# Kernel tuning notes

Measured on AMD Instinct MI355X. Metric: run time of the kernel, lower is better.

Reference implementation:

```python
import jax, jax.numpy as jnp
import numpy as np

H = 8  # number of heads


def setup_inputs() -> dict:
    key = jax.random.key(0)
    ks = jax.random.split(key, 7)
    B, L, D = 4, 2048, 512
    dh = D // H
    s = 1.0 / np.sqrt(D).astype(np.float32)
    return {
        "q": jax.random.normal(ks[0], (B, L, D), jnp.float32),
        "k": jax.random.normal(ks[1], (B, L, D), jnp.float32),
        "v": jax.random.normal(ks[2], (B, L, D), jnp.float32),
        "Wq": jax.random.normal(ks[3], (D, D), jnp.float32) * s,
        "Wk": jax.random.normal(ks[4], (D, D), jnp.float32) * s,
        "Wv": jax.random.normal(ks[5], (D, D), jnp.float32) * s,
        "E": jax.random.normal(ks[6], (L, dh), jnp.float32) * s,
    }


def _skew(QE):
    # QE: [B, H, L, L] -> pad one column on the left, reshape to [B,H,L+1,L],
    # drop the first row: the classic Music Transformer skewing trick.
    B, h, L, M = QE.shape
    padded = jnp.pad(QE, ((0, 0), (0, 0), (0, 0), (1, 0)))
    return padded.reshape(B, h, M + 1, L)[:, :, 1:, :]


def reference(q, k, v, Wq, Wk, Wv, E):
    B, L, D = q.shape
    dh = D // H

    def heads(x, W):
        return jnp.einsum('bld,de->ble', x, W).reshape(B, L, H, dh).transpose(0, 2, 1, 3)

    qh = heads(q, Wq)  # [B,H,L,dh]
    kh = heads(k, Wk)
    vh = heads(v, Wv)

    QE = jnp.einsum('bhld,md->bhlm', qh, E)      # [B,H,L,L]
    Srel = _skew(QE)                             # [B,H,L,L]
    QKt = jnp.einsum('bhld,bhmd->bhlm', qh, kh)  # [B,H,L,L]

    # NOTE: original divides AFTER softmax (faithful to source).
    attn = jax.nn.softmax(QKt + Srel, axis=-1) / float(np.sqrt(dh))
    out = jnp.einsum('bhlm,bhmd->bhld', attn, vh)
    return out.transpose(0, 2, 1, 3).reshape(B, L, D)
```

## Files before the change

### kernel.cpp

```cpp
#include <hip/hip_runtime.h>
#include <hip/hip_bf16.h>
#include <math.h>

typedef _Float16 f16;
typedef __attribute__((ext_vector_type(8))) _Float16 f16x8;
typedef __attribute__((ext_vector_type(4))) _Float16 f16x4;
typedef __attribute__((ext_vector_type(4))) float f32x4;

namespace {
constexpr int B = 4, L = 2048, D = 512, NH = 8, DH = 64;
}

__device__ __forceinline__ float dpp_xor1(float x) {
    return __int_as_float(__builtin_amdgcn_update_dpp(0, __float_as_int(x), 0xB1, 0xF, 0xF, true));
}
__device__ __forceinline__ float dpp_xor2(float x) {
    return __int_as_float(__builtin_amdgcn_update_dpp(0, __float_as_int(x), 0x4E, 0xF, 0xF, true));
}
__device__ __forceinline__ float dpp_ror4(float x) {
    return __int_as_float(__builtin_amdgcn_update_dpp(0, __float_as_int(x), 0x124, 0xF, 0xF, true));
}
__device__ __forceinline__ float dpp_ror8(float x) {
    return __int_as_float(__builtin_amdgcn_update_dpp(0, __float_as_int(x), 0x128, 0xF, 0xF, true));
}

__global__ __launch_bounds__(256)
void ecast_kernel(const float* __restrict__ E, f16* __restrict__ Ef) {
    int i4 = (blockIdx.x * 256 + threadIdx.x) * 4;
    float4 x = *(const float4*)(E + i4);
    *(f16x4*)(Ef + i4) = (f16x4){(f16)x.x, (f16)x.y, (f16)x.z, (f16)x.w};
}

__global__ __launch_bounds__(256)
void xcast_kernel(const float* __restrict__ q, const float* __restrict__ k,
                  const float* __restrict__ v, f16* __restrict__ Xf) {
    const int sel = blockIdx.y;
    const float* X = (sel == 0) ? q : (sel == 1) ? k : v;
    const size_t i4 = ((size_t)blockIdx.x * 256 + threadIdx.x) * 4;
    float4 x = *(const float4*)(X + i4);
    *(f16x4*)(Xf + (size_t)sel * ((size_t)B * L * D) + i4) =
        (f16x4){(f16)x.x, (f16)x.y, (f16)x.z, (f16)x.w};
}

__global__ __launch_bounds__(256)
void wtrans_kernel(const float* __restrict__ Wq, const float* __restrict__ Wk,
                   const float* __restrict__ Wv, f16* __restrict__ Wt) {
    __shared__ f16 Ws[64 * 65];
    const int sel = blockIdx.z;
    const float* W = (sel == 0) ? Wq : (sel == 1) ? Wk : Wv;
    f16* Wo = Wt + (size_t)sel * D * D;
    const int k0 = blockIdx.x * 64, n0 = blockIdx.y * 64;
    const int t = threadIdx.x;
#pragma unroll
    for (int i = 0; i < 16; ++i) {
        int idx = 256 * i + t;
        int r = idx >> 6, c = idx & 63;
        Ws[r * 65 + c] = (f16)W[(size_t)(k0 + r) * D + n0 + c];
    }
    __syncthreads();
    const int c = t >> 2, kseg = t & 3;
    f16x8 r0, r1;
#pragma unroll
    for (int j = 0; j < 8; ++j) r0[j] = Ws[(kseg * 16 + j) * 65 + c];
#pragma unroll
    for (int j = 0; j < 8; ++j) r1[j] = Ws[(kseg * 16 + 8 + j) * 65 + c];
    f16* o = Wo + (size_t)(n0 + c) * D + k0 + kseg * 16;
    *(f16x8*)o = r0;
    *(f16x8*)(o + 8) = r1;
}

__global__ __launch_bounds__(256, 4)
void proj_gemm(const f16* __restrict__ Xf, const f16* __restrict__ Wt,
               f16* __restrict__ Qf, f16* __restrict__ Kf, f16* __restrict__ Vtf) {
    __shared__ f16 As[128 * 72];
    __shared__ f16 Bs[64 * 72];
    const int flat = blockIdx.x;
    const int wg = (flat & 7) * 192 + (flat >> 3);
    const int by = wg % 24, bx = wg / 24;
    const int sel = by >> 3, h = by & 7;
    const int m0 = bx * 128;
    const f16* X = Xf + (size_t)sel * ((size_t)B * L * D);
    const f16* Bt = Wt + (size_t)sel * D * D + (size_t)h * 64 * D;
    const int t = threadIdx.x, wid = t >> 6, lane = t & 63;
    const int quad = lane >> 4, col = lane & 15;
    const int mw = wid * 32;

    f32x4 acc[2][4];
#pragma unroll
    for (int i = 0; i < 2; ++i)
#pragma unroll
        for (int j = 0; j < 4; ++j) acc[i][j] = (f32x4){0.f, 0.f, 0.f, 0.f};

    f16x8 xa[4];
    f16x8 breg[2];
    auto loadG = [&](int k0) {
#pragma unroll
        for (int i = 0; i < 4; ++i) {
            int idx = 256 * i + t;
            int r = idx >> 3, ch = idx & 7;
            xa[i] = *(const f16x8*)(X + (size_t)(m0 + r) * D + k0 + ch * 8);
        }
#pragma unroll
        for (int i = 0; i < 2; ++i) {
            int idx = 256 * i + t;
            int r = idx >> 3, ch = idx & 7;
            breg[i] = *(const f16x8*)(Bt + (size_t)r * D + k0 + ch * 8);
        }
    };
    auto storeL = [&]() {
#pragma unroll
        for (int i = 0; i < 4; ++i) {
            int idx = 256 * i + t;
            int r = idx >> 3, ch = idx & 7;
            *(f16x8*)(As + r * 72 + ch * 8) = xa[i];
        }
#pragma unroll
        for (int i = 0; i < 2; ++i) {
            int idx = 256 * i + t;
            int r = idx >> 3, ch = idx & 7;
            *(f16x8*)(Bs + r * 72 + ch * 8) = breg[i];
        }
    };

    loadG(0);
    for (int k0 = 0; k0 < D; k0 += 64) {
        __syncthreads();
        storeL();
        __syncthreads();
        if (k0 + 64 < D) loadG(k0 + 64);
#pragma unroll
        for (int ks = 0; ks < 2; ++ks) {
            f16x8 af[2], bf[4];
#pragma unroll
            for (int mt = 0; mt < 2; ++mt)
                af[mt] = *(const f16x8*)(As + (mw + mt * 16 + col) * 72 + quad * 8 + ks * 32);
#pragma unroll
            for (int nt = 0; nt < 4; ++nt)
                bf[nt] = *(const f16x8*)(Bs + (nt * 16 + col) * 72 + quad * 8 + ks * 32);
#pragma unroll
            for (int mt = 0; mt < 2; ++mt)
#pragma unroll
                for (int nt = 0; nt < 4; ++nt)
                    acc[mt][nt] = __builtin_amdgcn_mfma_f32_16x16x32_f16(af[mt], bf[nt], acc[mt][nt], 0, 0, 0);
        }
    }

    if (sel < 2) {
        f16* Y = (sel == 0) ? Qf : Kf;
#pragma unroll
        for (int mt = 0; mt < 2; ++mt)
#pragma unroll
            for (int nt = 0; nt < 4; ++nt)
#pragma unroll
                for (int reg = 0; reg < 4; ++reg) {
                    int m = m0 + mw + mt * 16 + quad * 4 + reg;
                    int bb = m >> 11, l = m & 2047, d = nt * 16 + col;
                    Y[((size_t)(bb * NH + h) * L + l) * DH + d] = (f16)acc[mt][nt][reg];
                }
    } else {
        __syncthreads();
        f16* Cs = As;
#pragma unroll
        for (int mt = 0; mt < 2; ++mt)
#pragma unroll
            for (int nt = 0; nt < 4; ++nt)
#pragma unroll
                for (int reg = 0; reg < 4; ++reg) {
                    int d = nt * 16 + col;
                    int lc = mw + mt * 16 + quad * 4 + reg;
                    Cs[d * 136 + lc] = (f16)acc[mt][nt][reg];
                }
        __syncthreads();
        const int dd = t >> 2, seg = t & 3;
        const int bb = m0 >> 11, l0 = m0 & 2047;
        f16* Yv = Vtf + ((size_t)(bb * NH + h) * DH + dd) * L + l0 + seg * 32;
#pragma unroll
        for (int j = 0; j < 4; ++j)
            *(f16x8*)(Yv + j * 8) = *(const f16x8*)(Cs + dd * 136 + seg * 32 + j * 8);
    }
}

__global__ __launch_bounds__(256, 4)
void attn_kernel(const f16* __restrict__ Qf, const f16* __restrict__ Kf,
                 const f16* __restrict__ Vtf, const f16* __restrict__ Ef,
                 float* __restrict__ out) {
    __shared__ f16 KfS[64 * 72];
    __shared__ f16 VfS[64 * 72];
    __shared__ f16 Pbuf[4][16 * 72];

    const int t = threadIdx.x, wid = t >> 6, lane = t & 63;
    const int quad = lane >> 4, col = lane & 15;
    const int l0w = blockIdx.x * 64 + wid * 16;
    const int h = blockIdx.y, bb = blockIdx.z;
    const size_t head = (size_t)(bb * NH + h) * (size_t)(L * DH);
    const f16* qf = Qf + head;
    const f16* kf = Kf + head;
    const f16* vt = Vtf + head;
    f16* Pw = Pbuf[wid];

    const f16x8 ones8 = {(f16)1.f, (f16)1.f, (f16)1.f, (f16)1.f,
                         (f16)1.f, (f16)1.f, (f16)1.f, (f16)1.f};

    f16x8 qF[2], qS[2];
    {
        const int m = l0w + col;
        const int mS = min(m + 1, L - 1);
#pragma unroll
        for (int ks = 0; ks < 2; ++ks) {
            const int off = quad * 8 + ks * 32;
            qF[ks] = *(const f16x8*)(qf + (size_t)m * DH + off);
            qS[ks] = *(const f16x8*)(qf + (size_t)mS * DH + off);
        }
    }

    f16x8 kreg[2], vreg[2];
    auto loadKV = [&](int c0) {
#pragma unroll
        for (int i = 0; i < 2; ++i) {
            int idx = 256 * i + t;
            int r = idx >> 3, ch = idx & 7;
            kreg[i] = *(const f16x8*)(kf + (size_t)(c0 + r) * DH + ch * 8);
            vreg[i] = *(const f16x8*)(vt + (size_t)r * L + c0 + ch * 8);
        }
    };

    f32x4 O[4];
#pragma unroll
    for (int i = 0; i < 4; ++i) O[i] = (f32x4){0.f, 0.f, 0.f, 0.f};
    f32x4 sacc = (f32x4){0.f, 0.f, 0.f, 0.f};
    float mrow[4] = {-1e30f, -1e30f, -1e30f, -1e30f};

    loadKV(0);
    for (int c0 = 0; c0 < L; c0 += 64) {
        __syncthreads();
#pragma unroll
        for (int i = 0; i < 2; ++i) {
            int idx = 256 * i + t;
            int r = idx >> 3, ch = idx & 7;
            *(f16x8*)(KfS + r * 72 + ch * 8) = kreg[i];
            *(f16x8*)(VfS + r * 72 + ch * 8) = vreg[i];
        }
        __syncthreads();
        if (c0 + 64 < L) loadKV(c0 + 64);

        const int d0 = c0 - l0w;

        f32x4 S[4];
        __builtin_amdgcn_s_setprio(1);
#pragma unroll
        for (int ns = 0; ns < 4; ++ns) {
            S[ns] = (f32x4){0.f, 0.f, 0.f, 0.f};
#pragma unroll
            for (int ks = 0; ks < 2; ++ks) {
                f16x8 bh = *(const f16x8*)(KfS + (ns * 16 + col) * 72 + quad * 8 + ks * 32);
                S[ns] = __builtin_amdgcn_mfma_f32_16x16x32_f16(qF[ks], bh, S[ns], 0, 0, 0);
            }
        }
        __builtin_amdgcn_s_setprio(0);

        const bool doA = (d0 <= 15);
        const bool doB = (d0 >= -61);
        const bool needmask = (d0 >= -48) && (d0 <= 16);
#pragma unroll 1
        for (int pass = 0; pass < 2; ++pass) {
            if ((pass == 0 && !doA) || (pass == 1 && !doB)) continue;
            const int jbase = (pass == 0) ? (d0 + L - 16) : (d0 - 17);
            f32x4 G[5];
#pragma unroll
            for (int g = 0; g < 5; ++g) {
                int er = min(max(jbase + g * 16 + col, 0), L - 1);
                G[g] = (f32x4){0.f, 0.f, 0.f, 0.f};
                const size_t eb = (size_t)er * DH + quad * 8;
#pragma unroll
                for (int ks = 0; ks < 2; ++ks) {
                    f16x8 e8 = *(const f16x8*)(Ef + eb + ks * 32);
                    G[g] = __builtin_amdgcn_mfma_f32_16x16x32_f16(
                               (pass == 0) ? qF[ks] : qS[ks], e8, G[g], 0, 0, 0);
                }
            }
#pragma unroll
            for (int reg = 0; reg < 4; ++reg) {
                const int r  = quad * 4 + reg;
                const int jj = col - r + 15;
                const int src = quad * 16 + (jj & 15);
                const bool hs = (col >= 15 - r);
#pragma unroll
                for (int ns = 0; ns < 4; ++ns) {
                    float H = hs ? G[ns][reg] : G[ns + 1][reg];
                    float val = __shfl(H, src, 64);
                    const int rel = d0 + ns * 16 + col - r;
                    const bool use = !needmask ||
                                     ((pass == 0) ? (rel <= 0) : (rel >= 2));
                    if (use) S[ns][reg] += val;
                }
            }
        }

#pragma unroll
        for (int reg = 0; reg < 4; ++reg) {
            float tm = fmaxf(fmaxf(S[0][reg], S[1][reg]), fmaxf(S[2][reg], S[3][reg]));
            tm = fmaxf(tm, dpp_xor1(tm));
            tm = fmaxf(tm, dpp_xor2(tm));
            tm = fmaxf(tm, dpp_ror4(tm));
            tm = fmaxf(tm, dpp_ror8(tm));
            const float mnew  = fmaxf(mrow[reg], tm);
            const float alpha = __expf(mrow[reg] - mnew);
            mrow[reg] = mnew;
            sacc[reg] *= alpha;
            const int r = quad * 4 + reg;
#pragma unroll
            for (int ns = 0; ns < 4; ++ns) {
                float p = __expf(S[ns][reg] - mnew);
                O[ns][reg] *= alpha;
                Pw[r * 72 + ns * 16 + col] = (f16)p;
            }
        }

        f16x8 pA[2];
        pA[0] = *(const f16x8*)(Pw + col * 72 + quad * 8);
        pA[1] = *(const f16x8*)(Pw + col * 72 + 32 + quad * 8);
        __builtin_amdgcn_s_setprio(1);
        sacc = __builtin_amdgcn_mfma_f32_16x16x32_f16(pA[0], ones8, sacc, 0, 0, 0);
        sacc = __builtin_amdgcn_mfma_f32_16x16x32_f16(pA[1], ones8, sacc, 0, 0, 0);
#pragma unroll
        for (int ns = 0; ns < 4; ++ns) {
#pragma unroll
            for (int ks = 0; ks < 2; ++ks) {
                f16x8 v8 = *(const f16x8*)(VfS + (ns * 16 + col) * 72 + quad * 8 + ks * 32);
                O[ns] = __builtin_amdgcn_mfma_f32_16x16x32_f16(pA[ks], v8, O[ns], 0, 0, 0);
            }
        }
        __builtin_amdgcn_s_setprio(0);
    }

#pragma unroll
    for (int reg = 0; reg < 4; ++reg) {
        const int l = l0w + quad * 4 + reg;
        const float inv = 1.0f / (sacc[reg] * 8.0f);
        float* o = out + ((size_t)bb * L + l) * D + h * DH;
#pragma unroll
        for (int ns = 0; ns < 4; ++ns)
            o[ns * 16 + col] = O[ns][reg] * inv;
    }
}

extern "C" void kernel_launch(void* const* d_in, const int* in_sizes, int n_in,
                              void* d_out, int out_size, void* d_ws, size_t ws_size,
                              hipStream_t stream) {
    const float* q  = (const float*)d_in[0];
    const float* k  = (const float*)d_in[1];
    const float* v  = (const float*)d_in[2];
    const float* Wq = (const float*)d_in[3];
    const float* Wk = (const float*)d_in[4];
    const float* Wv = (const float*)d_in[5];
    const float* E  = (const float*)d_in[6];
    float* out = (float*)d_out;

    const size_t plane = (size_t)B * NH * L * DH;
    f16* Qf  = (f16*)d_ws;
    f16* Kfp = Qf + plane;
    f16* Vtf = Kfp + plane;
    f16* Wt  = Vtf + plane;
    f16* Ef  = Wt + (size_t)3 * D * D;
    f16* Xf  = Ef + (size_t)L * DH;

    ecast_kernel<<<L * DH / 1024, 256, 0, stream>>>(E, Ef);
    xcast_kernel<<<dim3((unsigned)(plane / 1024), 3), 256, 0, stream>>>(q, k, v, Xf);
    wtrans_kernel<<<dim3(8, 8, 3), 256, 0, stream>>>(Wq, Wk, Wv, Wt);
    proj_gemm<<<dim3(1536), 256, 0, stream>>>(Xf, Wt, Qf, Kfp, Vtf);
    attn_kernel<<<dim3(L / 64, NH, B), 256, 0, stream>>>(Qf, Kfp, Vtf, Ef, out);
}
```

Measured before the change: 328.9 us.

## Widen projection GEMM tiles to 128x128 and skew relative logits via LDS

```diff
diff --git a/kernel.cpp b/kernel.cpp
--- a/kernel.cpp
+++ b/kernel.cpp
@@ -69,41 +69,37 @@
     *(f16x8*)(o + 8) = r1;
 }
 
-__global__ __launch_bounds__(256, 4)
+__global__ __launch_bounds__(256, 3)
 void proj_gemm(const f16* __restrict__ Xf, const f16* __restrict__ Wt,
                f16* __restrict__ Qf, f16* __restrict__ Kf, f16* __restrict__ Vtf) {
-    __shared__ f16 As[128 * 72];
-    __shared__ f16 Bs[64 * 72];
+    __shared__ f16 Sh[2 * 128 * 72];
+    f16* As = Sh;
+    f16* Bs = Sh + 128 * 72;
     const int flat = blockIdx.x;
-    const int wg = (flat & 7) * 192 + (flat >> 3);
-    const int by = wg % 24, bx = wg / 24;
-    const int sel = by >> 3, h = by & 7;
+    const int wg = (flat & 7) * 96 + (flat >> 3);
+    const int by = wg % 12, bx = wg / 12;
+    const int sel = by >> 2, hp = by & 3;
     const int m0 = bx * 128;
     const f16* X = Xf + (size_t)sel * ((size_t)B * L * D);
-    const f16* Bt = Wt + (size_t)sel * D * D + (size_t)h * 64 * D;
+    const f16* Bt = Wt + (size_t)sel * D * D + (size_t)hp * 128 * D;
     const int t = threadIdx.x, wid = t >> 6, lane = t & 63;
     const int quad = lane >> 4, col = lane & 15;
-    const int mw = wid * 32;
-
-    f32x4 acc[2][4];
-#pragma unroll
-    for (int i = 0; i < 2; ++i)
+    const int wr = wid >> 1, wc = wid & 1;
+    const int mw = wr * 64, nw = wc * 64;
+
+    f32x4 acc[4][4];
+#pragma unroll
+    for (int i = 0; i < 4; ++i)
 #pragma unroll
         for (int j = 0; j < 4; ++j) acc[i][j] = (f32x4){0.f, 0.f, 0.f, 0.f};
 
-    f16x8 xa[4];
-    f16x8 breg[2];
+    f16x8 xa[4], breg[4];
     auto loadG = [&](int k0) {
 #pragma unroll
         for (int i = 0; i < 4; ++i) {
             int idx = 256 * i + t;
             int r = idx >> 3, ch = idx & 7;
-            xa[i] = *(const f16x8*)(X + (size_t)(m0 + r) * D + k0 + ch * 8);
-        }
-#pragma unroll
-        for (int i = 0; i < 2; ++i) {
-            int idx = 256 * i + t;
-            int r = idx >> 3, ch = idx & 7;
+            xa[i]   = *(const f16x8*)(X  + (size_t)(m0 + r) * D + k0 + ch * 8);
             breg[i] = *(const f16x8*)(Bt + (size_t)r * D + k0 + ch * 8);
         }
     };
@@ -113,11 +109,6 @@
             int idx = 256 * i + t;
             int r = idx >> 3, ch = idx & 7;
             *(f16x8*)(As + r * 72 + ch * 8) = xa[i];
-        }
-#pragma unroll
-        for (int i = 0; i < 2; ++i) {
-            int idx = 256 * i + t;
-            int r = idx >> 3, ch = idx & 7;
             *(f16x8*)(Bs + r * 72 + ch * 8) = breg[i];
         }
     };
@@ -130,15 +121,15 @@
         if (k0 + 64 < D) loadG(k0 + 64);
 #pragma unroll
         for (int ks = 0; ks < 2; ++ks) {
-            f16x8 af[2], bf[4];
-#pragma unroll
-            for (int mt = 0; mt < 2; ++mt)
+            f16x8 af[4], bf[4];
+#pragma unroll
+            for (int mt = 0; mt < 4; ++mt)
                 af[mt] = *(const f16x8*)(As + (mw + mt * 16 + col) * 72 + quad * 8 + ks * 32);
 #pragma unroll
             for (int nt = 0; nt < 4; ++nt)
-                bf[nt] = *(const f16x8*)(Bs + (nt * 16 + col) * 72 + quad * 8 + ks * 32);
-#pragma unroll
-            for (int mt = 0; mt < 2; ++mt)
+                bf[nt] = *(const f16x8*)(Bs + (nw + nt * 16 + col) * 72 + quad * 8 + ks * 32);
+#pragma unroll
+            for (int mt = 0; mt < 4; ++mt)
 #pragma unroll
                 for (int nt = 0; nt < 4; ++nt)
                     acc[mt][nt] = __builtin_amdgcn_mfma_f32_16x16x32_f16(af[mt], bf[nt], acc[mt][nt], 0, 0, 0);
@@ -147,8 +138,9 @@
 
     if (sel < 2) {
         f16* Y = (sel == 0) ? Qf : Kf;
-#pragma unroll
-        for (int mt = 0; mt < 2; ++mt)
+        const int h = hp * 2 + wc;
+#pragma unroll
+        for (int mt = 0; mt < 4; ++mt)
 #pragma unroll
             for (int nt = 0; nt < 4; ++nt)
 #pragma unroll
@@ -159,24 +151,26 @@
                 }
     } else {
         __syncthreads();
-        f16* Cs = As;
-#pragma unroll
-        for (int mt = 0; mt < 2; ++mt)
+        f16* Cs = Sh;
+#pragma unroll
+        for (int mt = 0; mt < 4; ++mt)
 #pragma unroll
             for (int nt = 0; nt < 4; ++nt)
 #pragma unroll
                 for (int reg = 0; reg < 4; ++reg) {
-                    int d = nt * 16 + col;
+                    int dd = nt * 16 + col;
+                    int row = dd * 2 + wc;
                     int lc = mw + mt * 16 + quad * 4 + reg;
-                    Cs[d * 136 + lc] = (f16)acc[mt][nt][reg];
-                }
-        __syncthreads();
-        const int dd = t >> 2, seg = t & 3;
+                    Cs[row * 132 + lc] = (f16)acc[mt][nt][reg];
+                }
+        __syncthreads();
+        const int row2 = t >> 1, half = t & 1;
+        const int dd = row2 >> 1, hh = hp * 2 + (row2 & 1);
         const int bb = m0 >> 11, l0 = m0 & 2047;
-        f16* Yv = Vtf + ((size_t)(bb * NH + h) * DH + dd) * L + l0 + seg * 32;
-#pragma unroll
-        for (int j = 0; j < 4; ++j)
-            *(f16x8*)(Yv + j * 8) = *(const f16x8*)(Cs + dd * 136 + seg * 32 + j * 8);
+        f16* Yv = Vtf + ((size_t)(bb * NH + hh) * DH + dd) * L + l0 + half * 64;
+#pragma unroll
+        for (int j = 0; j < 8; ++j)
+            *(f16x8*)(Yv + j * 8) = *(const f16x8*)(Cs + row2 * 132 + half * 64 + j * 8);
     }
 }
 
@@ -186,7 +180,7 @@
                  float* __restrict__ out) {
     __shared__ f16 KfS[64 * 72];
     __shared__ f16 VfS[64 * 72];
-    __shared__ f16 Pbuf[4][16 * 72];
+    __shared__ float Gbuf[4][16 * 85];
 
     const int t = threadIdx.x, wid = t >> 6, lane = t & 63;
     const int quad = lane >> 4, col = lane & 15;
@@ -196,7 +190,8 @@
     const f16* qf = Qf + head;
     const f16* kf = Kf + head;
     const f16* vt = Vtf + head;
-    f16* Pw = Pbuf[wid];
+    float* Gw = Gbuf[wid];
+    f16* Pw = (f16*)Gw;
 
     const f16x8 ones8 = {(f16)1.f, (f16)1.f, (f16)1.f, (f16)1.f,
                          (f16)1.f, (f16)1.f, (f16)1.f, (f16)1.f};
@@ -279,19 +274,30 @@
                 }
             }
 #pragma unroll
-            for (int reg = 0; reg < 4; ++reg) {
-                const int r  = quad * 4 + reg;
-                const int jj = col - r + 15;
-                const int src = quad * 16 + (jj & 15);
-                const bool hs = (col >= 15 - r);
-#pragma unroll
-                for (int ns = 0; ns < 4; ++ns) {
-                    float H = hs ? G[ns][reg] : G[ns + 1][reg];
-                    float val = __shfl(H, src, 64);
-                    const int rel = d0 + ns * 16 + col - r;
-                    const bool use = !needmask ||
-                                     ((pass == 0) ? (rel <= 0) : (rel >= 2));
-                    if (use) S[ns][reg] += val;
+            for (int g = 0; g < 5; ++g)
+#pragma unroll
+                for (int reg = 0; reg < 4; ++reg)
+                    Gw[(quad * 4 + reg) * 85 + g * 16 + col] = G[g][reg];
+            if (!needmask) {
+#pragma unroll
+                for (int reg = 0; reg < 4; ++reg) {
+                    const int r = quad * 4 + reg;
+                    const float* gr = Gw + r * 85 + col - r + 15;
+#pragma unroll
+                    for (int ns = 0; ns < 4; ++ns)
+                        S[ns][reg] += gr[ns * 16];
+                }
+            } else {
+#pragma unroll
+                for (int reg = 0; reg < 4; ++reg) {
+                    const int r = quad * 4 + reg;
+                    const float* gr = Gw + r * 85 + col - r + 15;
+#pragma unroll
+                    for (int ns = 0; ns < 4; ++ns) {
+                        const int rel = d0 + ns * 16 + col - r;
+                        const bool use = (pass == 0) ? (rel <= 0) : (rel >= 2);
+                        if (use) S[ns][reg] += gr[ns * 16];
+                    }
                 }
             }
         }
@@ -367,6 +373,6 @@
     ecast_kernel<<<L * DH / 1024, 256, 0, stream>>>(E, Ef);
     xcast_kernel<<<dim3((unsigned)(plane / 1024), 3), 256, 0, stream>>>(q, k, v, Xf);
     wtrans_kernel<<<dim3(8, 8, 3), 256, 0, stream>>>(Wq, Wk, Wv, Wt);
-    proj_gemm<<<dim3(1536), 256, 0, stream>>>(Xf, Wt, Qf, Kfp, Vtf);
+    proj_gemm<<<dim3(768), 256, 0, stream>>>(Xf, Wt, Qf, Kfp, Vtf);
     attn_kernel<<<dim3(L / 64, NH, B), 256, 0, stream>>>(Qf, Kfp, Vtf, Ef, out);
 }
```

New measurement: 325.2 us. Within noise of the previous version (-1.1%).
